# Kernel tuning notes

Hardware: AMD Instinct MI355X
Metric: run time of the kernel (lower is better)

## Reference

```python
import jax, jax.numpy as jnp
import numpy as np

B, T, S, H, N = 4, 1024, 1024, 1024, 16
D = H // N
EPS = 1e-12
MASK_FILL = -1e6


def setup_inputs() -> dict:
    key = jax.random.key(0)
    ks = jax.random.split(key, 20)
    w = lambda i: jax.random.normal(ks[i], (H, H), jnp.float32) * 0.02
    zb = jnp.zeros((H,), jnp.float32)
    tgt_mask = jnp.tile(jnp.tril(jnp.ones((T, T), jnp.int32))[None], (B, 1, 1))
    return {
        "encoder_states": jax.random.normal(ks[0], (B, S, H), jnp.float32),
        "decoder_inputs": jax.random.normal(ks[1], (B, T, H), jnp.float32),
        "src_attn_mask": jnp.ones((B, S), jnp.int32),
        "tgt_attn_mask": tgt_mask,
        "q_w": w(2), "q_b": zb,
        "k_w": w(3), "k_b": zb,
        "v_w": w(4), "v_b": zb,
        "sq_w": w(5), "sq_b": zb,
        "sk_w": w(6), "sk_b": zb,
        "sv_w": w(7), "sv_b": zb,
        "dense_w": w(8), "dense_b": zb,
        "ln_g": jnp.ones((H,), jnp.float32),
        "ln_b": zb,
    }


def _layernorm(x, g, b):
    mu = jnp.mean(x, -1, keepdims=True)
    var = jnp.mean(jnp.square(x - mu), -1, keepdims=True)
    return (x - mu) * jax.lax.rsqrt(var + EPS) * g + b


def _attention(q, k, v, mask, dense_w, dense_b, ln_g, ln_b):
    # q:[B,Q,H] k,v:[B,K,H]; NOTE: original applies NO 1/sqrt(d) scaling.
    b, qlen, _ = q.shape
    klen = k.shape[1]
    qh = q.reshape(b, qlen, N, D).transpose(0, 2, 1, 3)  # [B,N,Q,D]
    kh = k.reshape(b, klen, N, D).transpose(0, 2, 1, 3)
    vh = v.reshape(b, klen, N, D).transpose(0, 2, 1, 3)
    scores = jnp.einsum('bnqd,bnkd->bnqk', qh, kh)
    m = mask.reshape(b, 1, qlen, klen) if mask.ndim == 3 else mask.reshape(b, 1, 1, klen)
    scores = jnp.where(m == 0, jnp.asarray(MASK_FILL, scores.dtype), scores)
    probs = jax.nn.softmax(scores, axis=-1)  # dropout = identity at eval
    ctx = jnp.einsum('bnqk,bnkd->bqnd', probs, vh)  # [B,Q,N,D]
    w = dense_w.T.reshape(N, D, H)
    proj = jnp.einsum('bqnd,ndh->bqh', ctx, w) + dense_b
    # Residual is q (the query projection), faithful to the original code.
    return _layernorm(q + proj, ln_g, ln_b)


def reference(encoder_states, decoder_inputs, src_attn_mask, tgt_attn_mask,
              q_w, q_b, k_w, k_b, v_w, v_b,
              sq_w, sq_b, sk_w, sk_b, sv_w, sv_b,
              dense_w, dense_b, ln_g, ln_b):
    lin = lambda x, w, b: x @ w.T + b
    # self-attention over decoder inputs
    q = lin(decoder_inputs, q_w, q_b)
    k = lin(decoder_inputs, k_w, k_b)
    v = lin(decoder_inputs, v_w, v_b)
    self_out = _attention(q, k, v, tgt_attn_mask, dense_w, dense_b, ln_g, ln_b)
    # cross-attention into encoder states (same dense/LayerNorm modules)
    q2 = lin(self_out, sq_w, sq_b)
    k2 = lin(encoder_states, sk_w, sk_b)
    v2 = lin(encoder_states, sv_w, sv_b)
    return _attention(q2, k2, v2, src_attn_mask, dense_w, dense_b, ln_g, ln_b)
```

## Files before the change

### kernel.cpp

```cpp
#include <hip/hip_runtime.h>

typedef __attribute__((ext_vector_type(4))) float f32x4;
typedef __attribute__((ext_vector_type(8))) short bf16x8;

#define GVOID const __attribute__((address_space(1))) void
#define LVOID __attribute__((address_space(3))) void

#define LOG2E 1.44269504f
#define LN2   0.69314718f

__device__ __forceinline__ float bf2f(ushort u){
  union { float f; unsigned int i; } c; c.i = ((unsigned int)u) << 16; return c.f;
}
__device__ __forceinline__ ushort f2bf(float f){
  union { float f; unsigned int i; } c; c.f = f;
  unsigned int r = (c.i + 0x7FFFu + ((c.i >> 16) & 1u)) >> 16;
  return (ushort)r;
}

struct CvtArgs {
  const float* s[9];
  ushort*      d[9];
  int          blks[9];
};
__global__ __launch_bounds__(256) void cvtk_multi(CvtArgs ca){
  int bid = blockIdx.x;
  int seg = 0, base = 0;
  while (bid - base >= ca.blks[seg]){ base += ca.blks[seg]; ++seg; }
  int i = ((bid - base) * 256 + threadIdx.x) * 4;
  float4 v = *(const float4*)(ca.s[seg] + i);
  ushort4 o;
  o.x = f2bf(v.x); o.y = f2bf(v.y); o.z = f2bf(v.z); o.w = f2bf(v.w);
  *(ushort4*)(ca.d[seg] + i) = o;
}

struct GemmArgs {
  const ushort* A[3];
  const ushort* W[3];
  const float*  bias[3];
  const ushort* R[3];
  ushort*       C[3];
  int           mode[3];
  float         scale[3];
};

__global__ __launch_bounds__(256,3) void gemm128r(GemmArgs ga, int nmat, int K){
  __shared__ ushort AS[3][128 * 32];
  __shared__ ushort BS[3][128 * 32];
  const int ntn = 8;
  const int per = ntn * nmat;
  const int x = blockIdx.x & 7, ii = blockIdx.x >> 3;
  const int gpx = (gridDim.x >> 3) / per;
  const int tm = x * gpx + ii / per;
  const int tq = ii % per;
  const int g = tq / ntn, tn = tq % ntn;
  const ushort* __restrict__ A = ga.A[g];
  const ushort* __restrict__ W = ga.W[g];
  const float*  __restrict__ bias = ga.bias[g];
  ushort* __restrict__ C = ga.C[g];
  const int mode = ga.mode[g];
  const float scale = ga.scale[g];

  const int t = threadIdx.x, lane = t & 63, wave = t >> 6;
  const int wr = wave >> 1, wc = wave & 1;
  const int l15 = lane & 15, l4 = lane >> 4;
  const int rowBase = tm * 128, colBase = tn * 128;

  auto stage = [&](int T, int slot){
    const int k0 = T << 5;
#pragma unroll
    for (int i = 0; i < 2; ++i){
      int cb = i * 256 + t;
      int row = cb >> 2;
      int kc = (cb & 3) ^ ((row >> 1) & 3);
      const ushort* srcA = A + (size_t)(rowBase + row) * K + k0 + kc * 8;
      __builtin_amdgcn_global_load_lds((GVOID*)srcA, (LVOID*)(&AS[slot][cb * 8]), 16, 0, 0);
      const ushort* srcB = W + (size_t)(colBase + row) * K + k0 + kc * 8;
      __builtin_amdgcn_global_load_lds((GVOID*)srcB, (LVOID*)(&BS[slot][cb * 8]), 16, 0, 0);
    }
  };

  f32x4 acc[4][4] = {};
  const int NT = K >> 5;
  stage(0, 0); stage(1, 1);
  int slot = 0;
  for (int T = 0; T < NT; ++T){
    if (T + 2 < NT){
      int s2 = slot + 2; if (s2 >= 3) s2 -= 3;
      stage(T + 2, s2);
      asm volatile("s_waitcnt vmcnt(8)" ::: "memory");
    } else if (T + 1 < NT){
      asm volatile("s_waitcnt vmcnt(4)" ::: "memory");
    } else {
      asm volatile("s_waitcnt vmcnt(0)" ::: "memory");
    }
    __builtin_amdgcn_s_barrier();
    const ushort* As_ = &AS[slot][0];
    const ushort* Bs_ = &BS[slot][0];
    bf16x8 a[4], b[4];
#pragma unroll
    for (int m = 0; m < 4; ++m){
      int row = wr * 64 + m * 16 + l15;
      int ch = (row << 2) + (l4 ^ ((row >> 1) & 3));
      a[m] = *(const bf16x8*)(As_ + ch * 8);
    }
#pragma unroll
    for (int n = 0; n < 4; ++n){
      int row = wc * 64 + n * 16 + l15;
      int ch = (row << 2) + (l4 ^ ((row >> 1) & 3));
      b[n] = *(const bf16x8*)(Bs_ + ch * 8);
    }
#pragma unroll
    for (int m = 0; m < 4; ++m)
#pragma unroll
    for (int n = 0; n < 4; ++n)
      acc[m][n] = __builtin_amdgcn_mfma_f32_16x16x32_bf16(a[m], b[n], acc[m][n], 0, 0, 0);
    asm volatile("s_waitcnt lgkmcnt(0)" ::: "memory");
    __builtin_amdgcn_s_barrier();
    slot = slot == 2 ? 0 : slot + 1;
  }
#pragma unroll
  for (int m = 0; m < 4; ++m)
#pragma unroll
  for (int n = 0; n < 4; ++n){
    int colm = colBase + wc * 64 + n * 16 + l15;
    float bi = bias[colm];
#pragma unroll
    for (int r = 0; r < 4; ++r){
      int row = rowBase + wr * 64 + m * 16 + l4 * 4 + r;
      float v = (acc[m][n][r] + bi) * scale;
      if (mode == 2){
        int bb = row >> 10, tt = row & 1023, nh = colm >> 6, d = colm & 63;
        C[((size_t)((bb * 16 + nh) * 64 + d)) * 1024 + tt] = f2bf(v);
      } else {
        C[(size_t)row * 1024 + colm] = f2bf(v);
      }
    }
  }
}

__global__ __launch_bounds__(256,2) void gemm_bt(GemmArgs ga, int nmat, int M, int N, int K){
  __shared__ ushort As[2][128 * 64];
  __shared__ ushort Bs[2][64 * 64];
  const int nb = gridDim.x;
  const int ntn = N >> 6;
  const int tq_cnt = ntn * nmat;
  const int x = blockIdx.x & 7, ii = blockIdx.x >> 3;
  const int ipx = nb >> 3;
  const int gpx = ipx / tq_cnt;
  const int tm = x * gpx + ii / tq_cnt;
  const int tq = ii % tq_cnt;
  const int g = tq / ntn, tn = tq % ntn;
  const ushort* __restrict__ A = ga.A[g];
  const ushort* __restrict__ W = ga.W[g];
  const float*  __restrict__ bias = ga.bias[g];
  const ushort* __restrict__ R = ga.R[g];
  ushort* __restrict__ C = ga.C[g];
  const int mode = ga.mode[g];
  const float scale = ga.scale[g];

  const int t = threadIdx.x, lane = t & 63, wave = t >> 6;
  const int wr = wave >> 1, wc = wave & 1;
  const int l15 = lane & 15, l4 = lane >> 4;
  const int rowBase = tm * 128, colBase = tn * 64;

  auto stage = [&](int buf, int k0){
#pragma unroll
    for (int j = 0; j < 4; ++j){
      int cb = j * 256 + wave * 64;
      int p = cb + lane;
      int row = p >> 3;
      int kc = (p & 7) ^ (row & 7);
      const ushort* src = A + (size_t)(rowBase + row) * K + k0 + kc * 8;
      __builtin_amdgcn_global_load_lds((GVOID*)src, (LVOID*)(&As[buf][cb * 8]), 16, 0, 0);
    }
#pragma unroll
    for (int j = 0; j < 2; ++j){
      int cb = j * 256 + wave * 64;
      int p = cb + lane;
      int row = p >> 3;
      int kc = (p & 7) ^ (row & 7);
      const ushort* src = W + (size_t)(colBase + row) * K + k0 + kc * 8;
      __builtin_amdgcn_global_load_lds((GVOID*)src, (LVOID*)(&Bs[buf][cb * 8]), 16, 0, 0);
    }
  };

  f32x4 acc[4][2] = {};
  const int NT = K >> 6;
  stage(0, 0);
  __syncthreads();
  for (int tk = 0; tk < NT; ++tk){
    const int cur = tk & 1;
    if (tk + 1 < NT) stage(cur ^ 1, (tk + 1) * 64);
#pragma unroll
    for (int kk = 0; kk < 2; ++kk){
      bf16x8 a[4], b[2];
#pragma unroll
      for (int m = 0; m < 4; ++m){
        int row = wr * 64 + m * 16 + l15;
        int ch = row * 8 + kk * 4 + l4;
        ch ^= (row & 7);
        a[m] = *(const bf16x8*)(&As[cur][ch * 8]);
      }
#pragma unroll
      for (int n = 0; n < 2; ++n){
        int row = wc * 32 + n * 16 + l15;
        int ch = row * 8 + kk * 4 + l4;
        ch ^= (row & 7);
        b[n] = *(const bf16x8*)(&Bs[cur][ch * 8]);
      }
#pragma unroll
      for (int m = 0; m < 4; ++m)
#pragma unroll
      for (int n = 0; n < 2; ++n)
        acc[m][n] = __builtin_amdgcn_mfma_f32_16x16x32_bf16(a[m], b[n], acc[m][n], 0, 0, 0);
    }
    __syncthreads();
  }
#pragma unroll
  for (int m = 0; m < 4; ++m)
#pragma unroll
  for (int n = 0; n < 2; ++n)
#pragma unroll
  for (int r = 0; r < 4; ++r){
    int row = rowBase + wr * 64 + m * 16 + l4 * 4 + r;
    int col = colBase + wc * 32 + n * 16 + l15;
    float v = (acc[m][n][r] + bias[col]) * scale;
    if (mode == 1) v += bf2f(R[(size_t)row * N + col]) * LN2;
    C[(size_t)row * N + col] = f2bf(v);
  }
}

__global__ __launch_bounds__(256,4) void attn_kernel(const ushort* __restrict__ Q, const ushort* __restrict__ Kv,
    const ushort* __restrict__ Vt, ushort* __restrict__ O, const int* __restrict__ smask, int causal){
  __shared__ ushort Ks[2][64 * 64];
  __shared__ ushort Vs[2][64 * 64];
  __shared__ __align__(16) char Ps[4][2048];
  const int p = blockIdx.x;
  const int x = p & 7, j = p >> 3;
  const int gg = x * 8 + (j & 7);
  const int b = gg >> 4, head = gg & 15;
  const int rr = j >> 3;
  int qt;
  if (causal){
    int lo = rr & 3, hi = rr >> 2;
    qt = (hi == 0) ? lo * 2 : (hi == 1) ? lo * 2 + 1 : (hi == 2) ? 15 - lo * 2 : 14 - lo * 2;
  } else qt = rr;
  const int t = threadIdx.x, lane = t & 63, wave = t >> 6;
  const int l15 = lane & 15, l4 = lane >> 4;
  const int qr0 = qt * 64 + wave * 16;
  const int sw = (l15 & 7) << 3;

  bf16x8 aq[2];
#pragma unroll
  for (int kk = 0; kk < 2; ++kk)
    aq[kk] = *(const bf16x8*)(Q + (size_t)(b * 1024 + qr0 + l15) * 1024 + head * 64 + kk * 32 + l4 * 8);

  f32x4 cacc[4] = {};
  float mrow = -1e30f, lrow = 0.f;

  auto stage = [&](int buf, int k0){
#pragma unroll
    for (int jj = 0; jj < 2; ++jj){
      int cb = jj * 256 + wave * 64;
      int pp = cb + lane;
      int row = pp >> 3;
      int kc = (pp & 7) ^ (row & 7);
      const ushort* src = Kv + (size_t)(b * 1024 + k0 + row) * 1024 + head * 64 + kc * 8;
      __builtin_amdgcn_global_load_lds((GVOID*)src, (LVOID*)(&Ks[buf][cb * 8]), 16, 0, 0);
    }
#pragma unroll
    for (int jj = 0; jj < 2; ++jj){
      int cb = jj * 256 + wave * 64;
      int pp = cb + lane;
      int row = pp >> 3;
      int kc = (pp & 7) ^ (row & 7);
      const ushort* src = Vt + (size_t)((b * 16 + head) * 64 + row) * 1024 + k0 + kc * 8;
      __builtin_amdgcn_global_load_lds((GVOID*)src, (LVOID*)(&Vs[buf][cb * 8]), 16, 0, 0);
    }
  };

  const int nkt = causal ? (qt + 1) : 16;
  stage(0, 0);
  __syncthreads();
  char* Pb = &Ps[wave][0];
  for (int kt = 0; kt < nkt; ++kt){
    const int cur = kt & 1;
    const int k0 = kt * 64;
    if (kt + 1 < nkt) stage(cur ^ 1, (kt + 1) * 64);
    const ushort* Kb_ = &Ks[cur][0];
    const ushort* Vb_ = &Vs[cur][0];
    f32x4 st[4] = {};
#pragma unroll
    for (int kk = 0; kk < 2; ++kk){
      bf16x8 ak[4];
#pragma unroll
      for (int n = 0; n < 4; ++n){
        int row = n * 16 + l15;
        int ch = row * 8 + ((kk * 4 + l4) ^ (row & 7));
        ak[n] = *(const bf16x8*)(Kb_ + ch * 8);
      }
#pragma unroll
      for (int n = 0; n < 4; ++n)
        st[n] = __builtin_amdgcn_mfma_f32_16x16x32_bf16(ak[n], aq[kk], st[n], 0, 0, 0);
    }
    if (causal && k0 + 63 > qr0){
#pragma unroll
      for (int n = 0; n < 4; ++n)
#pragma unroll
      for (int r = 0; r < 4; ++r)
        if (k0 + n * 16 + l4 * 4 + r > qr0 + l15) st[n][r] = -1.5e6f;
    }
    if (smask){
#pragma unroll
      for (int n = 0; n < 4; ++n)
#pragma unroll
      for (int r = 0; r < 4; ++r){
        int mv = smask[b * 1024 + k0 + n * 16 + l4 * 4 + r];
        if (mv == 0) st[n][r] = -1.5e6f;
      }
    }
    float mx = st[0][0];
#pragma unroll
    for (int n = 0; n < 4; ++n)
#pragma unroll
    for (int r = 0; r < 4; ++r) mx = fmaxf(mx, st[n][r]);
    mx = fmaxf(mx, __shfl_xor(mx, 16));
    mx = fmaxf(mx, __shfl_xor(mx, 32));
    float mn = fmaxf(mrow, mx);
    float scal = __builtin_amdgcn_exp2f(mrow - mn);
    mrow = mn;
    float ps = 0.f;
#pragma unroll
    for (int n = 0; n < 4; ++n)
#pragma unroll
    for (int r = 0; r < 4; ++r){
      float pv = __builtin_amdgcn_exp2f(st[n][r] - mn);
      st[n][r] = pv;
      ps += pv;
    }
    ps += __shfl_xor(ps, 16);
    ps += __shfl_xor(ps, 32);
    lrow = lrow * scal + ps;
#pragma unroll
    for (int r = 0; r < 4; ++r){
      float sb = __shfl(scal, l4 * 4 + r);
#pragma unroll
      for (int nd = 0; nd < 4; ++nd) cacc[nd][r] *= sb;
    }
#pragma unroll
    for (int n = 0; n < 4; ++n){
      unsigned lo_, hi_;
      asm("v_cvt_pk_bf16_f32 %0, %1, %2" : "=v"(lo_) : "v"(st[n][0]), "v"(st[n][1]));
      asm("v_cvt_pk_bf16_f32 %0, %1, %2" : "=v"(hi_) : "v"(st[n][2]), "v"(st[n][3]));
      unsigned long long pk = (unsigned long long)lo_ | ((unsigned long long)hi_ << 32);
      *(unsigned long long*)(Pb + l15 * 128 + ((n * 32 + l4 * 8) ^ sw)) = pk;
    }
#pragma unroll
    for (int ks = 0; ks < 2; ++ks){
      bf16x8 bv[4];
#pragma unroll
      for (int nd = 0; nd < 4; ++nd){
        int row = nd * 16 + l15;
        int ch = row * 8 + ((ks * 4 + l4) ^ (row & 7));
        bv[nd] = *(const bf16x8*)(Vb_ + ch * 8);
      }
      int base = l15 * 128;
      int o = ks * 64 + l4 * 16;
      union { bf16x8 v; unsigned long long u[2]; } pa;
      pa.u[0] = *(const unsigned long long*)(Pb + base + ((o    ) ^ sw));
      pa.u[1] = *(const unsigned long long*)(Pb + base + ((o + 8) ^ sw));
#pragma unroll
      for (int nd = 0; nd < 4; ++nd)
        cacc[nd] = __builtin_amdgcn_mfma_f32_16x16x32_bf16(pa.v, bv[nd], cacc[nd], 0, 0, 0);
    }
    __syncthreads();
  }
#pragma unroll
  for (int r = 0; r < 4; ++r){
    float lb = __shfl(lrow, l4 * 4 + r);
    float inv = 1.f / lb;
    int row = qr0 + l4 * 4 + r;
#pragma unroll
    for (int nd = 0; nd < 4; ++nd){
      int col = head * 64 + nd * 16 + l15;
      O[(size_t)(b * 1024 + row) * 1024 + col] = f2bf(cacc[nd][r] * inv);
    }
  }
}

__global__ __launch_bounds__(256) void ln_kernel(const ushort* __restrict__ X, const float* __restrict__ g,
    const float* __restrict__ bta, ushort* __restrict__ outb, float* __restrict__ outf){
  const int row = blockIdx.x, t = threadIdx.x;
  const ushort* xr = X + (size_t)row * 1024;
  ushort4 u = *(const ushort4*)(xr + t * 4);
  float x0 = bf2f(u.x), x1 = bf2f(u.y), x2 = bf2f(u.z), x3 = bf2f(u.w);
  float s = x0 + x1 + x2 + x3;
  float s2 = x0 * x0 + x1 * x1 + x2 * x2 + x3 * x3;
#pragma unroll
  for (int d = 1; d < 64; d <<= 1){ s += __shfl_xor(s, d); s2 += __shfl_xor(s2, d); }
  __shared__ float red[8];
  const int lane = t & 63, wave = t >> 6;
  if (lane == 0){ red[wave] = s; red[4 + wave] = s2; }
  __syncthreads();
  s = red[0] + red[1] + red[2] + red[3];
  s2 = red[4] + red[5] + red[6] + red[7];
  float mu = s * (1.f / 1024.f);
  float var = fmaxf(s2 * (1.f / 1024.f) - mu * mu, 0.f);
  float rstd = rsqrtf(var + 1e-12f);
  int col = t * 4;
  float y0 = (x0 - mu) * rstd * g[col + 0] + bta[col + 0];
  float y1 = (x1 - mu) * rstd * g[col + 1] + bta[col + 1];
  float y2 = (x2 - mu) * rstd * g[col + 2] + bta[col + 2];
  float y3 = (x3 - mu) * rstd * g[col + 3] + bta[col + 3];
  if (outb){
    ushort4 o; o.x = f2bf(y0); o.y = f2bf(y1); o.z = f2bf(y2); o.w = f2bf(y3);
    *(ushort4*)(outb + (size_t)row * 1024 + col) = o;
  } else {
    float4 o; o.x = y0; o.y = y1; o.z = y2; o.w = y3;
    *(float4*)(outf + (size_t)row * 1024 + col) = o;
  }
}

extern "C" void kernel_launch(void* const* d_in, const int* in_sizes, int n_in,
                              void* d_out, int out_size, void* d_ws, size_t ws_size,
                              hipStream_t stream){
  const float* enc = (const float*)d_in[0];
  const float* dec = (const float*)d_in[1];
  const int* smask = (const int*)d_in[2];
  const float* q_w  = (const float*)d_in[4];  const float* q_b  = (const float*)d_in[5];
  const float* k_w  = (const float*)d_in[6];  const float* k_b  = (const float*)d_in[7];
  const float* v_w  = (const float*)d_in[8];  const float* v_b  = (const float*)d_in[9];
  const float* sq_w = (const float*)d_in[10]; const float* sq_b = (const float*)d_in[11];
  const float* sk_w = (const float*)d_in[12]; const float* sk_b = (const float*)d_in[13];
  const float* sv_w = (const float*)d_in[14]; const float* sv_b = (const float*)d_in[15];
  const float* dw   = (const float*)d_in[16]; const float* db   = (const float*)d_in[17];
  const float* lng  = (const float*)d_in[18]; const float* lnb  = (const float*)d_in[19];
  ushort* ws = (ushort*)d_ws;
  const size_t MEG = 1024u * 1024u;
  ushort* decb = ws + 0 * MEG;
  ushort* encb = ws + 4 * MEG;
  ushort* Qb   = ws + 8 * MEG;
  ushort* Kb   = ws + 12 * MEG;
  ushort* Vtb  = ws + 20 * MEG;
  ushort* ctx  = ws + 24 * MEG;
  ushort* S1   = ws + 28 * MEG;
  ushort* Wq  = ws + 32 * MEG; ushort* Wk  = ws + 33 * MEG; ushort* Wv  = ws + 34 * MEG;
  ushort* Wsq = ws + 35 * MEG; ushort* Wsk = ws + 36 * MEG; ushort* Wsv = ws + 37 * MEG;
  ushort* Wd  = ws + 38 * MEG;
  const int M = 4096, N = 1024, Kd = 1024;
  {
    CvtArgs ca;
    ca.s[0] = dec;  ca.d[0] = decb; ca.blks[0] = 4096;
    ca.s[1] = enc;  ca.d[1] = encb; ca.blks[1] = 4096;
    ca.s[2] = q_w;  ca.d[2] = Wq;   ca.blks[2] = 1024;
    ca.s[3] = k_w;  ca.d[3] = Wk;   ca.blks[3] = 1024;
    ca.s[4] = v_w;  ca.d[4] = Wv;   ca.blks[4] = 1024;
    ca.s[5] = sq_w; ca.d[5] = Wsq;  ca.blks[5] = 1024;
    ca.s[6] = sk_w; ca.d[6] = Wsk;  ca.blks[6] = 1024;
    ca.s[7] = sv_w; ca.d[7] = Wsv;  ca.blks[7] = 1024;
    ca.s[8] = dw;   ca.d[8] = Wd;   ca.blks[8] = 1024;
    cvtk_multi<<<15360, 256, 0, stream>>>(ca);
  }
  {
    GemmArgs ga = {};
    ga.A[0] = decb; ga.A[1] = decb; ga.A[2] = decb;
    ga.W[0] = Wq;   ga.W[1] = Wk;   ga.W[2] = Wv;
    ga.bias[0] = q_b; ga.bias[1] = k_b; ga.bias[2] = v_b;
    ga.C[0] = Qb;   ga.C[1] = Kb;   ga.C[2] = Vtb;
    ga.mode[0] = 0; ga.mode[1] = 0; ga.mode[2] = 2;
    ga.scale[0] = LOG2E; ga.scale[1] = 1.f; ga.scale[2] = 1.f;
    gemm128r<<<768, 256, 0, stream>>>(ga, 3, Kd);
  }
  attn_kernel<<<1024, 256, 0, stream>>>(Qb, Kb, Vtb, ctx, nullptr, 1);
  {
    GemmArgs ga = {};
    ga.A[0] = ctx; ga.W[0] = Wd; ga.bias[0] = db; ga.R[0] = Qb; ga.C[0] = S1; ga.mode[0] = 1;
    ga.scale[0] = 1.f;
    gemm_bt<<<512, 256, 0, stream>>>(ga, 1, M, N, Kd);
  }
  ln_kernel<<<4096, 256, 0, stream>>>(S1, lng, lnb, decb, nullptr);
  {
    GemmArgs ga = {};
    ga.A[0] = decb; ga.A[1] = encb; ga.A[2] = encb;
    ga.W[0] = Wsq;  ga.W[1] = Wsk;  ga.W[2] = Wsv;
    ga.bias[0] = sq_b; ga.bias[1] = sk_b; ga.bias[2] = sv_b;
    ga.C[0] = Qb;   ga.C[1] = Kb;   ga.C[2] = Vtb;
    ga.mode[0] = 0; ga.mode[1] = 0; ga.mode[2] = 2;
    ga.scale[0] = LOG2E; ga.scale[1] = 1.f; ga.scale[2] = 1.f;
    gemm128r<<<768, 256, 0, stream>>>(ga, 3, Kd);
  }
  attn_kernel<<<1024, 256, 0, stream>>>(Qb, Kb, Vtb, ctx, smask, 0);
  {
    GemmArgs ga = {};
    ga.A[0] = ctx; ga.W[0] = Wd; ga.bias[0] = db; ga.R[0] = Qb; ga.C[0] = S1; ga.mode[0] = 1;
    ga.scale[0] = 1.f;
    gemm_bt<<<512, 256, 0, stream>>>(ga, 1, M, N, Kd);
  }
  ln_kernel<<<4096, 256, 0, stream>>>(S1, lng, lnb, nullptr, (float*)d_out);
}
```

Measured before the change: 221.9 us.

## Replace 128x128 QKV GEMM with 256x256 tile ping-pong pipelined kernel

The fused QKV projection GEMM moves from 128x128 tiles with K=32 triple buffering to 256x256 tiles with K=64 double buffering. It uses 8 waves per block, and loads are split into quarter-tile stages interleaved with MFMA phases under sched_barrier/setprio control. The aim is higher arithmetic intensity per LDS/global byte and better overlap of loads with MFMA. The cost is 192 blocks, which is under one wave of blocks across 256 CUs, so occupancy is lower and some CUs sit idle. Register pressure from the 8x4 accumulators is also high.

```diff
diff --git a/kernel.cpp b/kernel.cpp
--- a/kernel.cpp
+++ b/kernel.cpp
@@ -44,10 +44,48 @@
   float         scale[3];
 };
 
-__global__ __launch_bounds__(256,3) void gemm128r(GemmArgs ga, int nmat, int K){
-  __shared__ ushort AS[3][128 * 32];
-  __shared__ ushort BS[3][128 * 32];
-  const int ntn = 8;
+#define PHASE(Abuf_, Bbuf_, MP, LOADB, DOSTAGE, ST_T, ST_BUF, ST_H, VMSTR)                      \
+  {                                                                                             \
+    __builtin_amdgcn_sched_barrier(0);                                                          \
+    bf16x8 a0k0, a0k1, a1k0, a1k1;                                                              \
+    { int row0 = wr * 128 + (MP) * 32 + l15;                                                    \
+      int row1 = row0 + 16;                                                                     \
+      a0k0 = *(const bf16x8*)((Abuf_) + row0 * 64 + (((    l4) ^ (row0 & 7)) * 8));             \
+      a0k1 = *(const bf16x8*)((Abuf_) + row0 * 64 + (((4 + l4) ^ (row0 & 7)) * 8));             \
+      a1k0 = *(const bf16x8*)((Abuf_) + row1 * 64 + (((    l4) ^ (row1 & 7)) * 8));             \
+      a1k1 = *(const bf16x8*)((Abuf_) + row1 * 64 + (((4 + l4) ^ (row1 & 7)) * 8));             \
+    }                                                                                           \
+    if (LOADB){                                                                                 \
+      _Pragma("unroll")                                                                         \
+      for (int n = 0; n < 4; ++n){                                                              \
+        int rowb = wc * 64 + n * 16 + l15;                                                      \
+        bfr[n][0] = *(const bf16x8*)((Bbuf_) + rowb * 64 + (((    l4) ^ (rowb & 7)) * 8));      \
+        bfr[n][1] = *(const bf16x8*)((Bbuf_) + rowb * 64 + (((4 + l4) ^ (rowb & 7)) * 8));      \
+      }                                                                                         \
+    }                                                                                           \
+    if (DOSTAGE) stageHalf(ST_T, ST_BUF, ST_H);                                                 \
+    __builtin_amdgcn_sched_barrier(0);                                                          \
+    __builtin_amdgcn_s_barrier();                                                               \
+    asm volatile("s_waitcnt lgkmcnt(0)" ::: "memory");                                          \
+    __builtin_amdgcn_sched_barrier(0);                                                          \
+    __builtin_amdgcn_s_setprio(1);                                                              \
+    _Pragma("unroll")                                                                           \
+    for (int n = 0; n < 4; ++n){                                                                \
+      acc[(MP)*2  ][n] = __builtin_amdgcn_mfma_f32_16x16x32_bf16(a0k0, bfr[n][0], acc[(MP)*2  ][n], 0,0,0); \
+      acc[(MP)*2  ][n] = __builtin_amdgcn_mfma_f32_16x16x32_bf16(a0k1, bfr[n][1], acc[(MP)*2  ][n], 0,0,0); \
+      acc[(MP)*2+1][n] = __builtin_amdgcn_mfma_f32_16x16x32_bf16(a1k0, bfr[n][0], acc[(MP)*2+1][n], 0,0,0); \
+      acc[(MP)*2+1][n] = __builtin_amdgcn_mfma_f32_16x16x32_bf16(a1k1, bfr[n][1], acc[(MP)*2+1][n], 0,0,0); \
+    }                                                                                           \
+    __builtin_amdgcn_s_setprio(0);                                                              \
+    __builtin_amdgcn_sched_barrier(0);                                                          \
+    asm volatile(VMSTR ::: "memory");                                                           \
+    __builtin_amdgcn_s_barrier();                                                               \
+  }
+
+__global__ __launch_bounds__(512,2) void gemm256p(GemmArgs ga, int nmat, int K){
+  __shared__ ushort AS[2][256 * 64];
+  __shared__ ushort BS[2][256 * 64];
+  const int ntn = 4;
   const int per = ntn * nmat;
   const int x = blockIdx.x & 7, ii = blockIdx.x >> 3;
   const int gpx = (gridDim.x >> 3) / per;
@@ -62,72 +100,61 @@
   const float scale = ga.scale[g];
 
   const int t = threadIdx.x, lane = t & 63, wave = t >> 6;
-  const int wr = wave >> 1, wc = wave & 1;
+  const int wr = wave >> 2, wc = wave & 3;
   const int l15 = lane & 15, l4 = lane >> 4;
-  const int rowBase = tm * 128, colBase = tn * 128;
-
-  auto stage = [&](int T, int slot){
-    const int k0 = T << 5;
-#pragma unroll
-    for (int i = 0; i < 2; ++i){
-      int cb = i * 256 + t;
-      int row = cb >> 2;
-      int kc = (cb & 3) ^ ((row >> 1) & 3);
-      const ushort* srcA = A + (size_t)(rowBase + row) * K + k0 + kc * 8;
-      __builtin_amdgcn_global_load_lds((GVOID*)srcA, (LVOID*)(&AS[slot][cb * 8]), 16, 0, 0);
-      const ushort* srcB = W + (size_t)(colBase + row) * K + k0 + kc * 8;
-      __builtin_amdgcn_global_load_lds((GVOID*)srcB, (LVOID*)(&BS[slot][cb * 8]), 16, 0, 0);
+  const int rowBase = tm * 256, colBase = tn * 256;
+
+  auto stageHalf = [&](int T, int buf, int h){
+    const int k0 = T << 6;
+    const int rowOff = (h & 1) << 7;
+    const bool isA = (h < 2);
+    const ushort* gbase = isA ? A : W;
+    const int grow = (isA ? rowBase : colBase) + rowOff;
+    ushort* lds = (isA ? &AS[buf][0] : &BS[buf][0]) + rowOff * 64;
+#pragma unroll
+    for (int i2 = 0; i2 < 2; ++i2){
+      int cb = i2 * 512 + t;
+      int row = cb >> 3;
+      int kc = (cb & 7) ^ (row & 7);
+      const ushort* src = gbase + (size_t)(grow + row) * K + k0 + kc * 8;
+      __builtin_amdgcn_global_load_lds((GVOID*)src, (LVOID*)(lds + cb * 8), 16, 0, 0);
     }
   };
 
-  f32x4 acc[4][4] = {};
-  const int NT = K >> 5;
-  stage(0, 0); stage(1, 1);
-  int slot = 0;
-  for (int T = 0; T < NT; ++T){
-    if (T + 2 < NT){
-      int s2 = slot + 2; if (s2 >= 3) s2 -= 3;
-      stage(T + 2, s2);
-      asm volatile("s_waitcnt vmcnt(8)" ::: "memory");
-    } else if (T + 1 < NT){
-      asm volatile("s_waitcnt vmcnt(4)" ::: "memory");
-    } else {
-      asm volatile("s_waitcnt vmcnt(0)" ::: "memory");
-    }
-    __builtin_amdgcn_s_barrier();
-    const ushort* As_ = &AS[slot][0];
-    const ushort* Bs_ = &BS[slot][0];
-    bf16x8 a[4], b[4];
-#pragma unroll
-    for (int m = 0; m < 4; ++m){
-      int row = wr * 64 + m * 16 + l15;
-      int ch = (row << 2) + (l4 ^ ((row >> 1) & 3));
-      a[m] = *(const bf16x8*)(As_ + ch * 8);
-    }
-#pragma unroll
-    for (int n = 0; n < 4; ++n){
-      int row = wc * 64 + n * 16 + l15;
-      int ch = (row << 2) + (l4 ^ ((row >> 1) & 3));
-      b[n] = *(const bf16x8*)(Bs_ + ch * 8);
-    }
-#pragma unroll
-    for (int m = 0; m < 4; ++m)
-#pragma unroll
-    for (int n = 0; n < 4; ++n)
-      acc[m][n] = __builtin_amdgcn_mfma_f32_16x16x32_bf16(a[m], b[n], acc[m][n], 0, 0, 0);
-    asm volatile("s_waitcnt lgkmcnt(0)" ::: "memory");
-    __builtin_amdgcn_s_barrier();
-    slot = slot == 2 ? 0 : slot + 1;
-  }
-#pragma unroll
-  for (int m = 0; m < 4; ++m)
+  f32x4 acc[8][4] = {};
+  bf16x8 bfr[4][2];
+  const ushort* A0 = &AS[0][0]; const ushort* A1 = &AS[1][0];
+  const ushort* B0 = &BS[0][0]; const ushort* B1 = &BS[1][0];
+  const int NT = K >> 6;
+  const int NI = NT >> 1;
+  stageHalf(0, 0, 2); stageHalf(0, 0, 3); stageHalf(0, 0, 0); stageHalf(0, 0, 1);
+  stageHalf(1, 1, 2); stageHalf(1, 1, 3);
+  asm volatile("s_waitcnt vmcnt(4)" ::: "memory");
+  __builtin_amdgcn_sched_barrier(0);
+  __builtin_amdgcn_s_barrier();
+  for (int i = 0; i < NI; ++i){
+    const int t1 = 2 * i + 1, t2 = 2 * i + 2, t3 = 2 * i + 3;
+    const bool nl = (t2 < NT);
+    PHASE(A0, B0, 0, 1, 1,  t1, 1, 0, "")
+    PHASE(A0, B0, 1, 0, 1,  t1, 1, 1, "")
+    PHASE(A0, B0, 2, 0, nl, t2, 0, 2, "")
+    if (nl){ PHASE(A0, B0, 3, 0, 1, t2, 0, 3, "s_waitcnt vmcnt(4)") }
+    else   { PHASE(A0, B0, 3, 0, 0, 0, 0, 0, "s_waitcnt vmcnt(0)") }
+    PHASE(A1, B1, 0, 1, nl, t2, 0, 0, "")
+    PHASE(A1, B1, 1, 0, nl, t2, 0, 1, "")
+    PHASE(A1, B1, 2, 0, nl, t3, 1, 2, "")
+    if (nl){ PHASE(A1, B1, 3, 0, 1, t3, 1, 3, "s_waitcnt vmcnt(4)") }
+    else   { PHASE(A1, B1, 3, 0, 0, 0, 0, 0, "") }
+  }
+#pragma unroll
+  for (int m = 0; m < 8; ++m)
 #pragma unroll
   for (int n = 0; n < 4; ++n){
     int colm = colBase + wc * 64 + n * 16 + l15;
     float bi = bias[colm];
 #pragma unroll
     for (int r = 0; r < 4; ++r){
-      int row = rowBase + wr * 64 + m * 16 + l4 * 4 + r;
+      int row = rowBase + wr * 128 + m * 16 + l4 * 4 + r;
       float v = (acc[m][n][r] + bi) * scale;
       if (mode == 2){
         int bb = row >> 10, tt = row & 1023, nh = colm >> 6, d = colm & 63;
@@ -470,7 +497,7 @@
     ga.C[0] = Qb;   ga.C[1] = Kb;   ga.C[2] = Vtb;
     ga.mode[0] = 0; ga.mode[1] = 0; ga.mode[2] = 2;
     ga.scale[0] = LOG2E; ga.scale[1] = 1.f; ga.scale[2] = 1.f;
-    gemm128r<<<768, 256, 0, stream>>>(ga, 3, Kd);
+    gemm256p<<<192, 512, 0, stream>>>(ga, 3, Kd);
   }
   attn_kernel<<<1024, 256, 0, stream>>>(Qb, Kb, Vtb, ctx, nullptr, 1);
   {
@@ -488,7 +515,7 @@
     ga.C[0] = Qb;   ga.C[1] = Kb;   ga.C[2] = Vtb;
     ga.mode[0] = 0; ga.mode[1] = 0; ga.mode[2] = 2;
     ga.scale[0] = LOG2E; ga.scale[1] = 1.f; ga.scale[2] = 1.f;
-    gemm128r<<<768, 256, 0, stream>>>(ga, 3, Kd);
+    gemm256p<<<192, 512, 0, stream>>>(ga, 3, Kd);
   }
   attn_kernel<<<1024, 256, 0, stream>>>(Qb, Kb, Vtb, ctx, smask, 0);
   {
```

After: 261.3 us. 1.18x slower.
